# Kernel optimization log

Hardware: AMD Instinct MI355X
Metric: run time of the kernel (lower is better)

The kernel has to match this reference:

```python
import jax, jax.numpy as jnp
import numpy as np

B, C, H, W = 4, 256, 48, 48
HEADS, DH = 8, 64
HID = HEADS * DH
EPS = 1e-5
SCALE = DH ** -0.5


def setup_inputs() -> dict:
    key = jax.random.key(0)
    ks = jax.random.split(key, 8)
    return {
        "tensor": jax.random.normal(ks[0], (B, C, H, W), jnp.float32),
        "norm_g": jnp.ones((C,), jnp.float32),                      # ChanLayerNorm gamma
        "w_qkv": jax.random.normal(ks[1], (3 * HID, C), jnp.float32) * 0.02,  # 1x1 conv, no bias
        "dw_q": jax.random.normal(ks[2], (HID, 1, 3, 3), jnp.float32) * 0.1,  # depthwise 3x3
        "dw_k": jax.random.normal(ks[3], (HID, 1, 3, 3), jnp.float32) * 0.1,
        "dw_v": jax.random.normal(ks[4], (HID, 1, 3, 3), jnp.float32) * 0.1,
        "w_out": jax.random.normal(ks[5], (C, HID), jnp.float32) * 0.02,      # 1x1 conv out
        "b_out": jnp.zeros((C,), jnp.float32),
    }


def _rope(t):
    # t: (b, h, s, d) -- rotary embedding over flattened spatial positions
    s, d = t.shape[-2], t.shape[-1]
    inv_freq = 1.0 / (10000.0 ** (jnp.arange(0, d, 2, dtype=jnp.float32) / d))
    freqs = jnp.arange(s, dtype=jnp.float32)[:, None] * inv_freq[None, :]     # (s, d/2)
    emb = jnp.concatenate([freqs, freqs], axis=-1)                            # (s, d)
    cos, sin = jnp.cos(emb), jnp.sin(emb)
    t1, t2 = t[..., : d // 2], t[..., d // 2 :]
    rot = jnp.concatenate([-t2, t1], axis=-1)
    return t * cos + rot * sin


def _dwconv(x, w):
    # depthwise 3x3, padding=1 (Primer conv), groups = channels
    return jax.lax.conv_general_dilated(
        x, w, window_strides=(1, 1), padding="SAME",
        feature_group_count=x.shape[1],
        dimension_numbers=("NCHW", "OIHW", "NCHW"))


def reference(tensor, norm_g, w_qkv, dw_q, dw_k, dw_v, w_out, b_out):
    x = tensor
    # ChanLayerNorm: normalize over channel dim
    mean = jnp.mean(x, axis=1, keepdims=True)
    var = jnp.var(x, axis=1, keepdims=True)
    xn = (x - mean) * jax.lax.rsqrt(var + EPS) * norm_g[None, :, None, None]
    # 1x1 conv to qkv
    qkv = jnp.einsum("bchw,oc->bohw", xn, w_qkv)
    q, k, v = jnp.split(qkv, 3, axis=1)
    q, k, v = _dwconv(q, dw_q), _dwconv(k, dw_k), _dwconv(v, dw_v)
    # b (h d) x y -> b h (x y) d
    def to_seq(t):
        b = t.shape[0]
        return t.reshape(b, HEADS, DH, H * W).transpose(0, 1, 3, 2)
    q, k, v = to_seq(q), to_seq(k), to_seq(v)
    q, k = _rope(q), _rope(k)
    q = q * SCALE
    sim = jnp.einsum("bhid,bhjd->bhij", q, k)
    attn = jax.nn.softmax(sim, axis=-1)
    out = jnp.einsum("bhij,bhjd->bhid", attn, v)
    # b h (x y) d -> b (h d) x y
    out = out.transpose(0, 1, 3, 2).reshape(out.shape[0], HID, H, W)
    return jnp.einsum("bchw,oc->bohw", out, w_out) + b_out[None, :, None, None]
```

## Files before the change

kernel.cpp:

```cpp
#include <hip/hip_runtime.h>
#include <math.h>

#define SS 2304
#define C_IN 256
#define HID 512
#define QKV3 1536
#define HEADS 8
#define DH 64
#define BATCH 4
#define EPSV 1e-5f
#define SCALEV 0.125f

typedef short s8v __attribute__((ext_vector_type(8)));
typedef float f4v __attribute__((ext_vector_type(4)));
typedef unsigned int u4v __attribute__((ext_vector_type(4)));
typedef unsigned int uint32;

static __device__ inline unsigned short f2bf(float x) {
    unsigned int u = __float_as_uint(x);
    u += 0x7fffu + ((u >> 16) & 1u);
    return (unsigned short)(u >> 16);
}
static __device__ inline float bf2f(unsigned short h) {
    return __uint_as_float((unsigned int)h << 16);
}
static __device__ inline f4v mm(s8v a, s8v b, f4v c) {
    return __builtin_amdgcn_mfma_f32_16x16x32_bf16(a, b, c, 0, 0, 0);
}
static __device__ inline s8v pk4(uint32 a, uint32 b, uint32 c, uint32 d) {
    u4v t; t[0] = a; t[1] = b; t[2] = c; t[3] = d;
    return __builtin_bit_cast(s8v, t);
}
static __device__ inline uint32 pk_rnd(float x) {
    unsigned int u = __float_as_uint(x);
    unsigned int uh = (u + (0x7fffu + ((u >> 16) & 1u))) & 0xffff0000u;
    float r = x - __uint_as_float(uh);
    return (uh >> 16) | (__float_as_uint(r) & 0xffff0000u);
}
static __device__ inline uint32 pk_trunc(float x) {
    unsigned int u = __float_as_uint(x);
    unsigned int h = u & 0xffff0000u;
    float r = x - __uint_as_float(h);
    return (h >> 16) | (__float_as_uint(r) & 0xffff0000u);
}
static __device__ inline uint32 rot16(uint32 u) { return (u >> 16) | (u << 16); }
static __device__ inline u4v rot16v(u4v u) {
    u4v r; r[0] = rot16(u[0]); r[1] = rot16(u[1]); r[2] = rot16(u[2]); r[3] = rot16(u[3]);
    return r;
}

__global__ void prep_wgint(const float* __restrict__ w, const float* __restrict__ g,
                           uint32* __restrict__ wgint, float* __restrict__ wsum) {
    __shared__ float red[256];
    int o = blockIdx.x, c = threadIdx.x;
    float v = w[o * C_IN + c] * g[c];
    wgint[o * C_IN + c] = pk_rnd(v);
    red[c] = v;
    __syncthreads();
    for (int st = 128; st > 0; st >>= 1) {
        if (c < st) red[c] += red[c + st];
        __syncthreads();
    }
    if (c == 0) wsum[o] = red[0];
}

__global__ void prep_woutint(const float* __restrict__ w, uint32* __restrict__ wi) {
    int idx = blockIdx.x * 256 + threadIdx.x;
    wi[idx] = pk_rnd(w[idx]);
}

__global__ void prep_rope(float* __restrict__ cosT, float* __restrict__ sinT) {
    int idx = blockIdx.x * 256 + threadIdx.x;
    if (idx >= SS * 32) return;
    int s = idx >> 5, f = idx & 31;
    double inv = pow(10000.0, -(double)f / 32.0);
    double ang = (double)s * inv;
    cosT[idx] = (float)cos(ang);
    sinT[idx] = (float)sin(ang);
}

__global__ void prep_stats(const float* __restrict__ x, float* __restrict__ mean,
                           float* __restrict__ rstd) {
    int p = blockIdx.x * 256 + threadIdx.x;
    int b = p / SS, s = p % SS;
    const float* xp = x + (size_t)b * C_IN * SS + s;
    float sm = 0.f;
    for (int c = 0; c < C_IN; ++c) sm += xp[(size_t)c * SS];
    float mu = sm * (1.0f / C_IN);
    float vs = 0.f;
    for (int c = 0; c < C_IN; ++c) { float d = xp[(size_t)c * SS] - mu; vs += d * d; }
    mean[p] = mu;
    rstd[p] = rsqrtf(vs * (1.0f / C_IN) + EPSV);
}

__global__ __launch_bounds__(256) void xt_pack(const float* __restrict__ x,
                                               uint32* __restrict__ xTint) {
    __shared__ float tile[64][65];
    int b = blockIdx.z;
    int c0 = blockIdx.y * 64;
    int s0 = blockIdx.x * 64;
    int t = threadIdx.x;
    int sl = t & 63, cg = t >> 6;
#pragma unroll
    for (int i = 0; i < 16; ++i) {
        int c = cg * 16 + i;
        tile[c][sl] = x[((size_t)b * C_IN + c0 + c) * SS + s0 + sl];
    }
    __syncthreads();
    int cl = t & 63, sg = t >> 6;
#pragma unroll
    for (int i = 0; i < 16; ++i) {
        int s = sg * 16 + i;
        xTint[((size_t)b * SS + s0 + s) * C_IN + c0 + cl] = pk_rnd(tile[cl][s]);
    }
}

__global__ __launch_bounds__(256, 4) void qkv_mfma(
    const uint32* __restrict__ wgint, const uint32* __restrict__ xTint,
    const float* __restrict__ wsum, const float* __restrict__ mean,
    const float* __restrict__ rstd, float* __restrict__ qkv) {
    int b = blockIdx.z;
    int m0 = blockIdx.y * 128;
    int n0 = blockIdx.x * 64;
    int t = threadIdx.x;
    int wv = t >> 6, lane = t & 63, l15 = lane & 15, quad = lane >> 4;
    int wm = wv * 32;
    const uint32* Ab = wgint + (size_t)(m0 + wm) * C_IN;
    const uint32* Bb = xTint + ((size_t)b * SS + n0) * C_IN;
    f4v acc[2][4];
#pragma unroll
    for (int mt = 0; mt < 2; ++mt)
#pragma unroll
        for (int nt = 0; nt < 4; ++nt) acc[mt][nt] = (f4v){0.f, 0.f, 0.f, 0.f};
    u4v af[2][2], bf[2][4];
    auto ldA = [&](int ch, u4v* A) {
#pragma unroll
        for (int mt = 0; mt < 2; ++mt)
            A[mt] = *(const u4v*)(Ab + (size_t)(mt * 16 + l15) * C_IN + ch * 16 + quad * 4);
    };
    auto ldB = [&](int ch, u4v* B) {
#pragma unroll
        for (int nt = 0; nt < 4; ++nt)
            B[nt] = *(const u4v*)(Bb + (size_t)(nt * 16 + l15) * C_IN + ch * 16 + quad * 4);
    };
    ldA(0, af[0]);
    ldB(0, bf[0]);
#pragma unroll 2
    for (int ch = 0; ch < 16; ++ch) {
        int cur = ch & 1, nxt = cur ^ 1;
        if (ch + 1 < 16) { ldA(ch + 1, af[nxt]); ldB(ch + 1, bf[nxt]); }
        u4v br[4];
#pragma unroll
        for (int nt = 0; nt < 4; ++nt) br[nt] = rot16v(bf[cur][nt]);
#pragma unroll
        for (int mt = 0; mt < 2; ++mt) {
            s8v a = __builtin_bit_cast(s8v, af[cur][mt]);
#pragma unroll
            for (int nt = 0; nt < 4; ++nt) {
                acc[mt][nt] = mm(a, __builtin_bit_cast(s8v, bf[cur][nt]), acc[mt][nt]);
                acc[mt][nt] = mm(a, __builtin_bit_cast(s8v, br[nt]), acc[mt][nt]);
            }
        }
    }
    float mnv[4], rsv[4];
#pragma unroll
    for (int nt = 0; nt < 4; ++nt) {
        int n = n0 + nt * 16 + l15;
        mnv[nt] = mean[b * SS + n];
        rsv[nt] = rstd[b * SS + n];
    }
#pragma unroll
    for (int mt = 0; mt < 2; ++mt)
#pragma unroll
        for (int r = 0; r < 4; ++r) {
            int m = m0 + wm + mt * 16 + quad * 4 + r;
            float ws = wsum[m];
            float* dst = qkv + ((size_t)b * QKV3 + m) * SS + n0 + l15;
#pragma unroll
            for (int nt = 0; nt < 4; ++nt)
                dst[nt * 16] = rsv[nt] * (acc[mt][nt][r] - mnv[nt] * ws);
        }
}

__global__ __launch_bounds__(256) void conv_rope(
    const float* __restrict__ qkv, const float* __restrict__ dwq,
    const float* __restrict__ dwk, const float* __restrict__ dwv,
    const float* __restrict__ cosT, const float* __restrict__ sinT,
    unsigned short* __restrict__ qhi, unsigned short* __restrict__ qlo,
    unsigned short* __restrict__ khi, unsigned short* __restrict__ klo,
    uint32* __restrict__ vtint) {
    __shared__ float tile[64][65];
    int b = blockIdx.z;
    int part = blockIdx.y >> 3;
    int h = blockIdx.y & 7;
    int s0 = blockIdx.x * 64;
    int t = threadIdx.x;
    int sl = t & 63, dgrp = t >> 6;
    int s = s0 + sl;
    int y = s / 48, xx = s - y * 48;
    int bh = b * HEADS + h;
    const float* dw = (part == 0) ? dwq : (part == 1) ? dwk : dwv;
#pragma unroll
    for (int i = 0; i < 16; ++i) {
        int d = dgrp * 16 + i;
        int cch = part * HID + h * DH + d;
        const float* src = qkv + ((size_t)b * QKV3 + cch) * SS;
        const float* wp = dw + (h * DH + d) * 9;
        float acc = 0.f;
#pragma unroll
        for (int dy = -1; dy <= 1; ++dy) {
            int yy = y + dy;
            if (yy < 0 || yy >= 48) continue;
#pragma unroll
            for (int dx = -1; dx <= 1; ++dx) {
                int xv = xx + dx;
                if (xv < 0 || xv >= 48) continue;
                acc += wp[(dy + 1) * 3 + (dx + 1)] * src[yy * 48 + xv];
            }
        }
        if (part == 2) {
            size_t o = ((size_t)bh * DH + d) * SS + s;
            vtint[o] = pk_rnd(acc);
        } else {
            tile[d][sl] = acc;
        }
    }
    if (part == 2) return;
    __syncthreads();
    int d2 = t & 63, srow = t >> 6;
    unsigned short* hiA = (part == 0) ? qhi : khi;
    unsigned short* loA = (part == 0) ? qlo : klo;
#pragma unroll
    for (int i = 0; i < 16; ++i) {
        int sp = srow + 4 * i;
        float v0 = tile[d2][sp];
        float vp = tile[d2 ^ 32][sp];
        int f = d2 & 31;
        float cv = cosT[(s0 + sp) * 32 + f];
        float sv = sinT[(s0 + sp) * 32 + f];
        float rot = (d2 < 32) ? -vp : vp;
        float val = v0 * cv + rot * sv;
        if (part == 0) val *= SCALEV;
        size_t o = ((size_t)bh * SS + s0 + sp) * DH + d2;
        unsigned short hu = f2bf(val);
        hiA[o] = hu;
        loA[o] = f2bf(val - bf2f(hu));
    }
}

__global__ __launch_bounds__(256, 2) void attn_mfma(
    const unsigned short* __restrict__ qhi, const unsigned short* __restrict__ qlo,
    const unsigned short* __restrict__ khi, const unsigned short* __restrict__ klo,
    const uint32* __restrict__ vtint,
    float* __restrict__ Opart, float* __restrict__ lpart) {
    __shared__ float lds[4][64][68];
    __shared__ float lsl[4][64];
    int bh = blockIdx.z;
    int jh = blockIdx.y;
    int i0 = blockIdx.x * 64;
    int t = threadIdx.x;
    int wv = t >> 6;
    int lane = t & 63;
    int l15 = lane & 15;
    int quad = lane >> 4;

    s8v qf[4][4];
#pragma unroll
    for (int ig = 0; ig < 4; ++ig) {
        size_t qb = ((size_t)bh * SS + i0 + ig * 16 + l15) * DH + quad * 8;
        qf[ig][0] = *(const s8v*)(qhi + qb);
        qf[ig][1] = *(const s8v*)(qhi + qb + 32);
        qf[ig][2] = *(const s8v*)(qlo + qb);
        qf[ig][3] = *(const s8v*)(qlo + qb + 32);
    }
    f4v oacc[4][4];
#pragma unroll
    for (int dt = 0; dt < 4; ++dt)
#pragma unroll
        for (int ig = 0; ig < 4; ++ig) oacc[dt][ig] = (f4v){0.f, 0.f, 0.f, 0.f};
    float lsum[4] = {0.f, 0.f, 0.f, 0.f};

    const size_t kbh = (size_t)bh * SS * DH;
    const uint32* vbase = vtint + (size_t)bh * DH * SS;
    const int jbase = jh * 1152 + wv * 16;

    s8v kc[2][4], vc[2][4];
    auto ldK = [&](int s, s8v* K) {
        size_t row = kbh + (size_t)(jbase + s * 64 + l15) * DH + quad * 8;
        K[0] = *(const s8v*)(khi + row);
        K[1] = *(const s8v*)(khi + row + 32);
        K[2] = *(const s8v*)(klo + row);
        K[3] = *(const s8v*)(klo + row + 32);
    };
    auto ldV = [&](int s, s8v* V) {
        size_t col = (size_t)(jbase + s * 64 + quad * 4);
#pragma unroll
        for (int dt = 0; dt < 4; ++dt)
            V[dt] = __builtin_bit_cast(
                s8v, *(const u4v*)(vbase + (size_t)(dt * 16 + l15) * SS + col));
    };
    ldK(0, kc[0]);
    ldV(0, vc[0]);
#pragma unroll 2
    for (int s = 0; s < 18; ++s) {
        int cur = s & 1, nxt = cur ^ 1;
        if (s + 1 < 18) { ldK(s + 1, kc[nxt]); ldV(s + 1, vc[nxt]); }
        f4v sv[4];
#pragma unroll
        for (int ig = 0; ig < 4; ++ig) {
            f4v sx = {0.f, 0.f, 0.f, 0.f};
            sx = mm(kc[cur][0], qf[ig][0], sx);
            sx = mm(kc[cur][1], qf[ig][1], sx);
            sx = mm(kc[cur][0], qf[ig][2], sx);
            sx = mm(kc[cur][1], qf[ig][3], sx);
            sx = mm(kc[cur][2], qf[ig][0], sx);
            sx = mm(kc[cur][3], qf[ig][1], sx);
            sv[ig] = sx;
        }
        s8v B1[4], B2[4];
#pragma unroll
        for (int ig = 0; ig < 4; ++ig) {
            float p0 = __expf(sv[ig][0]), p1 = __expf(sv[ig][1]);
            float p2 = __expf(sv[ig][2]), p3 = __expf(sv[ig][3]);
            lsum[ig] += (p0 + p1) + (p2 + p3);
            uint32 u0 = pk_trunc(p0), u1 = pk_trunc(p1);
            uint32 u2 = pk_trunc(p2), u3 = pk_trunc(p3);
            B1[ig] = pk4(u0, u1, u2, u3);
            B2[ig] = pk4(rot16(u0), rot16(u1), rot16(u2), rot16(u3));
        }
#pragma unroll
        for (int dt = 0; dt < 4; ++dt)
#pragma unroll
            for (int ig = 0; ig < 4; ++ig) {
                oacc[dt][ig] = mm(vc[cur][dt], B1[ig], oacc[dt][ig]);
                oacc[dt][ig] = mm(vc[cur][dt], B2[ig], oacc[dt][ig]);
            }
    }
#pragma unroll
    for (int ig = 0; ig < 4; ++ig) {
        float v = lsum[ig];
        v += __shfl_xor(v, 16);
        v += __shfl_xor(v, 32);
        if (quad == 0) lsl[wv][ig * 16 + l15] = v;
    }
#pragma unroll
    for (int dt = 0; dt < 4; ++dt)
#pragma unroll
        for (int ig = 0; ig < 4; ++ig)
#pragma unroll
            for (int r = 0; r < 4; ++r)
                lds[wv][dt * 16 + quad * 4 + r][ig * 16 + l15] = oacc[dt][ig][r];
    __syncthreads();
    int d = t >> 2, qg = (t & 3) * 16;
    size_t ob = (((size_t)jh * 32 + bh) * DH + d) * SS + i0 + qg;
#pragma unroll
    for (int j4 = 0; j4 < 4; ++j4) {
        float4 a0 = *(const float4*)&lds[0][d][qg + j4 * 4];
        float4 a1 = *(const float4*)&lds[1][d][qg + j4 * 4];
        float4 a2 = *(const float4*)&lds[2][d][qg + j4 * 4];
        float4 a3 = *(const float4*)&lds[3][d][qg + j4 * 4];
        float4 rr;
        rr.x = (a0.x + a1.x) + (a2.x + a3.x);
        rr.y = (a0.y + a1.y) + (a2.y + a3.y);
        rr.z = (a0.z + a1.z) + (a2.z + a3.z);
        rr.w = (a0.w + a1.w) + (a2.w + a3.w);
        *(float4*)(Opart + ob + j4 * 4) = rr;
    }
    if (t < 64) {
        float v = (lsl[0][t] + lsl[1][t]) + (lsl[2][t] + lsl[3][t]);
        lpart[((size_t)jh * 32 + bh) * SS + i0 + t] = v;
    }
}

__global__ __launch_bounds__(256) void combine_t(
    const float* __restrict__ Opart, const float* __restrict__ lpart,
    uint32* __restrict__ OTint) {
    __shared__ uint32 tile[64][65];
    int bh = blockIdx.y;
    int s0 = blockIdx.x * 64;
    int b = bh >> 3, h = bh & 7;
    int t = threadIdx.x;
    int sl = t & 63, dg = t >> 6;
    float linv = 1.f / (lpart[(size_t)bh * SS + s0 + sl] +
                        lpart[(size_t)(32 + bh) * SS + s0 + sl]);
#pragma unroll
    for (int i = 0; i < 16; ++i) {
        int d = dg * 16 + i;
        size_t off = ((size_t)bh * DH + d) * SS + s0 + sl;
        float v = (Opart[off] + Opart[off + (size_t)32 * DH * SS]) * linv;
        tile[d][sl] = pk_rnd(v);
    }
    __syncthreads();
    int dl = t & 63, sg = t >> 6;
#pragma unroll
    for (int i = 0; i < 16; ++i) {
        int s = sg * 16 + i;
        OTint[((size_t)b * SS + s0 + s) * HID + h * DH + dl] = tile[dl][s];
    }
}

__global__ __launch_bounds__(256, 4) void outproj_mfma(
    const uint32* __restrict__ OTint, const uint32* __restrict__ woutint,
    const float* __restrict__ b_out, float* __restrict__ out) {
    int b = blockIdx.z;
    int m0 = blockIdx.y * 32;
    int n0 = blockIdx.x * 128;
    int t = threadIdx.x;
    int wv = t >> 6, lane = t & 63, l15 = lane & 15, quad = lane >> 4;
    int wn = wv * 32;
    const uint32* Ab = woutint + (size_t)m0 * HID;
    const uint32* Bb = OTint + ((size_t)b * SS + n0 + wn) * HID;
    f4v acc[2][2];
#pragma unroll
    for (int mt = 0; mt < 2; ++mt)
#pragma unroll
        for (int nt = 0; nt < 2; ++nt) acc[mt][nt] = (f4v){0.f, 0.f, 0.f, 0.f};
    u4v af[2][2], bf[2][2];
    auto ldA = [&](int ch, u4v* A) {
#pragma unroll
        for (int mt = 0; mt < 2; ++mt)
            A[mt] = *(const u4v*)(Ab + (size_t)(mt * 16 + l15) * HID + ch * 16 + quad * 4);
    };
    auto ldB = [&](int ch, u4v* B) {
#pragma unroll
        for (int nt = 0; nt < 2; ++nt)
            B[nt] = *(const u4v*)(Bb + (size_t)(nt * 16 + l15) * HID + ch * 16 + quad * 4);
    };
    ldA(0, af[0]);
    ldB(0, bf[0]);
#pragma unroll 2
    for (int ch = 0; ch < 32; ++ch) {
        int cur = ch & 1, nxt = cur ^ 1;
        if (ch + 1 < 32) { ldA(ch + 1, af[nxt]); ldB(ch + 1, bf[nxt]); }
        u4v br[2];
#pragma unroll
        for (int nt = 0; nt < 2; ++nt) br[nt] = rot16v(bf[cur][nt]);
#pragma unroll
        for (int mt = 0; mt < 2; ++mt) {
            s8v a = __builtin_bit_cast(s8v, af[cur][mt]);
#pragma unroll
            for (int nt = 0; nt < 2; ++nt) {
                acc[mt][nt] = mm(a, __builtin_bit_cast(s8v, bf[cur][nt]), acc[mt][nt]);
                acc[mt][nt] = mm(a, __builtin_bit_cast(s8v, br[nt]), acc[mt][nt]);
            }
        }
    }
#pragma unroll
    for (int mt = 0; mt < 2; ++mt)
#pragma unroll
        for (int r = 0; r < 4; ++r) {
            int o = m0 + mt * 16 + quad * 4 + r;
            float bo = b_out[o];
            float* dst = out + ((size_t)b * C_IN + o) * SS + n0 + wn + l15;
#pragma unroll
            for (int nt = 0; nt < 2; ++nt) dst[nt * 16] = acc[mt][nt][r] + bo;
        }
}

extern "C" void kernel_launch(void* const* d_in, const int* in_sizes, int n_in,
                              void* d_out, int out_size, void* d_ws, size_t ws_size,
                              hipStream_t stream) {
    (void)in_sizes; (void)n_in; (void)out_size; (void)ws_size;
    const float* x     = (const float*)d_in[0];
    const float* g     = (const float*)d_in[1];
    const float* w_qkv = (const float*)d_in[2];
    const float* dwq   = (const float*)d_in[3];
    const float* dwk   = (const float*)d_in[4];
    const float* dwv   = (const float*)d_in[5];
    const float* w_out = (const float*)d_in[6];
    const float* b_out = (const float*)d_in[7];
    float* out = (float*)d_out;

    char* ws = (char*)d_ws;
    size_t off = 0;
    auto alloc = [&](size_t nbytes) -> void* {
        char* p = ws + off;
        off = (off + nbytes + 255) & ~(size_t)255;
        return (void*)p;
    };
    const size_t NSD = (size_t)BATCH * HEADS * SS * DH;
    uint32* wgint   = (uint32*)alloc((size_t)QKV3 * C_IN * 4);
    uint32* woutint = (uint32*)alloc((size_t)C_IN * HID * 4);
    float* wsum = (float*)alloc((size_t)QKV3 * 4);
    float* mean = (float*)alloc((size_t)BATCH * SS * 4);
    float* rstd = (float*)alloc((size_t)BATCH * SS * 4);
    float* cosT = (float*)alloc((size_t)SS * 32 * 4);
    float* sinT = (float*)alloc((size_t)SS * 32 * 4);
    float* qkv  = (float*)alloc((size_t)BATCH * QKV3 * SS * 4);
    unsigned short* qhi  = (unsigned short*)alloc(NSD * 2);
    unsigned short* qlo  = (unsigned short*)alloc(NSD * 2);
    unsigned short* khi  = (unsigned short*)alloc(NSD * 2);
    unsigned short* klo  = (unsigned short*)alloc(NSD * 2);
    uint32* vtint = (uint32*)alloc(NSD * 4);
    float* lpart = (float*)alloc((size_t)2 * 32 * SS * 4);
    uint32* xTint = (uint32*)qhi;
    float*  Opart = qkv;
    uint32* OTint = (uint32*)(qkv + 2 * NSD);

    prep_wgint<<<QKV3, 256, 0, stream>>>(w_qkv, g, wgint, wsum);
    prep_woutint<<<512, 256, 0, stream>>>(w_out, woutint);
    prep_rope<<<288, 256, 0, stream>>>(cosT, sinT);
    prep_stats<<<36, 256, 0, stream>>>(x, mean, rstd);
    xt_pack<<<dim3(36, 4, BATCH), 256, 0, stream>>>(x, xTint);
    qkv_mfma<<<dim3(36, 12, BATCH), 256, 0, stream>>>(wgint, xTint, wsum, mean, rstd, qkv);
    conv_rope<<<dim3(36, 24, BATCH), 256, 0, stream>>>(qkv, dwq, dwk, dwv, cosT, sinT,
                                                       qhi, qlo, khi, klo, vtint);
    attn_mfma<<<dim3(36, 2, 32), 256, 0, stream>>>(qhi, qlo, khi, klo, vtint,
                                                   Opart, lpart);
    combine_t<<<dim3(36, 32), 256, 0, stream>>>(Opart, lpart, OTint);
    outproj_mfma<<<dim3(18, 8, BATCH), 256, 0, stream>>>(OTint, woutint, b_out, out);
}
```

Measured before the change: 497.0 us.

## Fuse channel stats into transpose pack and halve attention LDS footprint

Measured after the change: 1.360 ms. 2.74x slower.

```diff
diff --git a/kernel.cpp b/kernel.cpp
--- a/kernel.cpp
+++ b/kernel.cpp
@@ -79,33 +79,29 @@
     sinT[idx] = (float)sin(ang);
 }
 
-__global__ void prep_stats(const float* __restrict__ x, float* __restrict__ mean,
-                           float* __restrict__ rstd) {
-    int p = blockIdx.x * 256 + threadIdx.x;
-    int b = p / SS, s = p % SS;
-    const float* xp = x + (size_t)b * C_IN * SS + s;
-    float sm = 0.f;
-    for (int c = 0; c < C_IN; ++c) sm += xp[(size_t)c * SS];
-    float mu = sm * (1.0f / C_IN);
-    float vs = 0.f;
-    for (int c = 0; c < C_IN; ++c) { float d = xp[(size_t)c * SS] - mu; vs += d * d; }
-    mean[p] = mu;
-    rstd[p] = rsqrtf(vs * (1.0f / C_IN) + EPSV);
-}
-
 __global__ __launch_bounds__(256) void xt_pack(const float* __restrict__ x,
-                                               uint32* __restrict__ xTint) {
+                                               uint32* __restrict__ xTint,
+                                               float* __restrict__ psum,
+                                               float* __restrict__ psq) {
     __shared__ float tile[64][65];
+    __shared__ float sred[4][64];
+    __shared__ float qred[4][64];
     int b = blockIdx.z;
     int c0 = blockIdx.y * 64;
     int s0 = blockIdx.x * 64;
     int t = threadIdx.x;
     int sl = t & 63, cg = t >> 6;
+    float ps = 0.f, pq = 0.f;
 #pragma unroll
     for (int i = 0; i < 16; ++i) {
         int c = cg * 16 + i;
-        tile[c][sl] = x[((size_t)b * C_IN + c0 + c) * SS + s0 + sl];
-    }
+        float v = x[((size_t)b * C_IN + c0 + c) * SS + s0 + sl];
+        tile[c][sl] = v;
+        ps += v;
+        pq += v * v;
+    }
+    sred[cg][sl] = ps;
+    qred[cg][sl] = pq;
     __syncthreads();
     int cl = t & 63, sg = t >> 6;
 #pragma unroll
@@ -113,6 +109,26 @@
         int s = sg * 16 + i;
         xTint[((size_t)b * SS + s0 + s) * C_IN + c0 + cl] = pk_rnd(tile[cl][s]);
     }
+    if (t < 64) {
+        float S = (sred[0][t] + sred[1][t]) + (sred[2][t] + sred[3][t]);
+        float Q = (qred[0][t] + qred[1][t]) + (qred[2][t] + qred[3][t]);
+        size_t o = (size_t)blockIdx.y * (BATCH * SS) + (size_t)b * SS + s0 + t;
+        psum[o] = S;
+        psq[o] = Q;
+    }
+}
+
+__global__ void finalize_stats(const float* __restrict__ psum,
+                               const float* __restrict__ psq,
+                               float* __restrict__ mean, float* __restrict__ rstd) {
+    int p = blockIdx.x * 256 + threadIdx.x;
+    const int NP = BATCH * SS;
+    float S = (psum[p] + psum[NP + p]) + (psum[2 * NP + p] + psum[3 * NP + p]);
+    float Q = (psq[p] + psq[NP + p]) + (psq[2 * NP + p] + psq[3 * NP + p]);
+    float mu = S * (1.0f / C_IN);
+    float var = Q * (1.0f / C_IN) - mu * mu;
+    mean[p] = mu;
+    rstd[p] = rsqrtf(var + EPSV);
 }
 
 __global__ __launch_bounds__(256, 4) void qkv_mfma(
@@ -248,12 +264,12 @@
     }
 }
 
-__global__ __launch_bounds__(256, 2) void attn_mfma(
+__global__ __launch_bounds__(256, 4) void attn_mfma(
     const unsigned short* __restrict__ qhi, const unsigned short* __restrict__ qlo,
     const unsigned short* __restrict__ khi, const unsigned short* __restrict__ klo,
     const uint32* __restrict__ vtint,
     float* __restrict__ Opart, float* __restrict__ lpart) {
-    __shared__ float lds[4][64][68];
+    __shared__ float lds[2][64][68];
     __shared__ float lsl[4][64];
     int bh = blockIdx.z;
     int jh = blockIdx.y;
@@ -343,13 +359,25 @@
         v += __shfl_xor(v, 32);
         if (quad == 0) lsl[wv][ig * 16 + l15] = v;
     }
-#pragma unroll
-    for (int dt = 0; dt < 4; ++dt)
-#pragma unroll
-        for (int ig = 0; ig < 4; ++ig)
-#pragma unroll
-            for (int r = 0; r < 4; ++r)
-                lds[wv][dt * 16 + quad * 4 + r][ig * 16 + l15] = oacc[dt][ig][r];
+    if (wv < 2) {
+#pragma unroll
+        for (int dt = 0; dt < 4; ++dt)
+#pragma unroll
+            for (int ig = 0; ig < 4; ++ig)
+#pragma unroll
+                for (int r = 0; r < 4; ++r)
+                    lds[wv][dt * 16 + quad * 4 + r][ig * 16 + l15] = oacc[dt][ig][r];
+    }
+    __syncthreads();
+    if (wv >= 2) {
+#pragma unroll
+        for (int dt = 0; dt < 4; ++dt)
+#pragma unroll
+            for (int ig = 0; ig < 4; ++ig)
+#pragma unroll
+                for (int r = 0; r < 4; ++r)
+                    lds[wv - 2][dt * 16 + quad * 4 + r][ig * 16 + l15] += oacc[dt][ig][r];
+    }
     __syncthreads();
     int d = t >> 2, qg = (t & 3) * 16;
     size_t ob = (((size_t)jh * 32 + bh) * DH + d) * SS + i0 + qg;
@@ -357,13 +385,11 @@
     for (int j4 = 0; j4 < 4; ++j4) {
         float4 a0 = *(const float4*)&lds[0][d][qg + j4 * 4];
         float4 a1 = *(const float4*)&lds[1][d][qg + j4 * 4];
-        float4 a2 = *(const float4*)&lds[2][d][qg + j4 * 4];
-        float4 a3 = *(const float4*)&lds[3][d][qg + j4 * 4];
         float4 rr;
-        rr.x = (a0.x + a1.x) + (a2.x + a3.x);
-        rr.y = (a0.y + a1.y) + (a2.y + a3.y);
-        rr.z = (a0.z + a1.z) + (a2.z + a3.z);
-        rr.w = (a0.w + a1.w) + (a2.w + a3.w);
+        rr.x = a0.x + a1.x;
+        rr.y = a0.y + a1.y;
+        rr.z = a0.z + a1.z;
+        rr.w = a0.w + a1.w;
         *(float4*)(Opart + ob + j4 * 4) = rr;
     }
     if (t < 64) {
@@ -484,6 +510,8 @@
     float* wsum = (float*)alloc((size_t)QKV3 * 4);
     float* mean = (float*)alloc((size_t)BATCH * SS * 4);
     float* rstd = (float*)alloc((size_t)BATCH * SS * 4);
+    float* psum = (float*)alloc((size_t)4 * BATCH * SS * 4);
+    float* psq  = (float*)alloc((size_t)4 * BATCH * SS * 4);
     float* cosT = (float*)alloc((size_t)SS * 32 * 4);
     float* sinT = (float*)alloc((size_t)SS * 32 * 4);
     float* qkv  = (float*)alloc((size_t)BATCH * QKV3 * SS * 4);
@@ -500,8 +528,8 @@
     prep_wgint<<<QKV3, 256, 0, stream>>>(w_qkv, g, wgint, wsum);
     prep_woutint<<<512, 256, 0, stream>>>(w_out, woutint);
     prep_rope<<<288, 256, 0, stream>>>(cosT, sinT);
-    prep_stats<<<36, 256, 0, stream>>>(x, mean, rstd);
-    xt_pack<<<dim3(36, 4, BATCH), 256, 0, stream>>>(x, xTint);
+    xt_pack<<<dim3(36, 4, BATCH), 256, 0, stream>>>(x, xTint, psum, psq);
+    finalize_stats<<<36, 256, 0, stream>>>(psum, psq, mean, rstd);
     qkv_mfma<<<dim3(36, 12, BATCH), 256, 0, stream>>>(wgint, xTint, wsum, mean, rstd, qkv);
     conv_rope<<<dim3(36, 24, BATCH), 256, 0, stream>>>(qkv, dwq, dwk, dwv, cosT, sinT,
                                                        qhi, qlo, khi, klo, vtint);
```
